# Kernel optimization log

Measured on AMD Instinct MI355X. Metric: run time of the kernel, lower is better.

The kernel has to match this reference:

```python
import jax, jax.numpy as jnp
import numpy as np

N_NODES = 100000
N_EDGES = 1200000
F_IN, F_HID, F_OUT = 128, 64, 40


def gcn_conv(x, W, b, src, dst, n):
    # PyG GCNConv: h = x @ W; add self-loops; symmetric norm; scatter-add; + bias
    h = x @ W  # [N, F]
    loops = jnp.arange(n)
    s = jnp.concatenate([src, loops])
    d = jnp.concatenate([dst, loops])
    deg = jnp.zeros((n,), x.dtype).at[d].add(jnp.asarray(1.0, x.dtype))
    dis = jax.lax.rsqrt(deg)  # deg >= 1 thanks to self-loops
    norm = dis[s] * dis[d]  # [E+N]
    msg = h[s] * norm[:, None]  # gather + scale
    out = jnp.zeros((n, h.shape[1]), x.dtype).at[d].add(msg)  # scatter-add
    return out + b


def setup_inputs() -> dict:
    key = jax.random.key(0)
    ks = jax.random.split(key, 8)
    sc = lambda f: 1.0 / np.sqrt(f)
    return {
        "x": jax.random.normal(ks[0], (N_NODES, F_IN), jnp.float32),
        "edge_index": jax.random.randint(ks[1], (2, N_EDGES), 0, N_NODES, jnp.int64),
        "W1": jax.random.normal(ks[2], (F_IN, F_HID), jnp.float32) * sc(F_IN),
        "b1": jnp.zeros((F_HID,), jnp.float32),
        "W2": jax.random.normal(ks[3], (F_HID, F_HID), jnp.float32) * sc(F_HID),
        "b2": jnp.zeros((F_HID,), jnp.float32),
        "W3": jax.random.normal(ks[4], (F_HID, F_OUT), jnp.float32) * sc(F_HID),
        "b3": jnp.zeros((F_OUT,), jnp.float32),
    }


def reference(x, edge_index, W1, b1, W2, b2, W3, b3):
    src, dst = edge_index[0], edge_index[1]
    n = x.shape[0]
    h = jax.nn.relu(gcn_conv(x, W1, b1, src, dst, n))  # dropout is identity (eval)
    h = jax.nn.relu(gcn_conv(h, W2, b2, src, dst, n))
    out = gcn_conv(h, W3, b3, src, dst, n)
    return jax.nn.log_softmax(out, axis=1)
```

## Files before the change

### kernel.cpp

```cpp
#include <hip/hip_runtime.h>
#include <math.h>


static inline int cdiv(long a, int b) { return (int)((a + b - 1) / b); }

__device__ __forceinline__ unsigned short f2bf(float f) {
    unsigned u = __float_as_uint(f);
    u += 0x7fffu + ((u >> 16) & 1u);
    return (unsigned short)(u >> 16);
}
__device__ __forceinline__ float bf2f(unsigned short b) {
    return __uint_as_float(((unsigned)b) << 16);
}

typedef float floatx2 __attribute__((ext_vector_type(2)));
typedef short bf16x8  __attribute__((ext_vector_type(8)));
typedef float f32x4   __attribute__((ext_vector_type(4)));
__device__ __forceinline__ float4 fp8x4_f(unsigned u) {
    floatx2 lo = __builtin_amdgcn_cvt_pk_f32_fp8(u, false);
    floatx2 hi = __builtin_amdgcn_cvt_pk_f32_fp8(u, true);
    float4 r; r.x = lo[0]; r.y = lo[1]; r.z = hi[0]; r.w = hi[1];
    return r;
}
__device__ __forceinline__ unsigned char f_fp8(float v) {
    return (unsigned char)(__builtin_amdgcn_cvt_pk_fp8_f32(v, v, 0u, false) & 0xFFu);
}

#define RSH 9
#define RNODES 512
#define GB 1024
#define NBMAX 256
#define SMASK 0x1FFFF
#define PSLACK (RNODES * 16)
#define EBMAX 12288

__global__ __launch_bounds__(256)
void k_bhist(const int* __restrict__ dst, int* __restrict__ bh,
             int E, int NB, int EPB) {
    __shared__ int bcnt[NBMAX];
    const int tid = threadIdx.x, blk = blockIdx.x;
    for (int i = tid; i < NB; i += 256) bcnt[i] = 0;
    __syncthreads();
    const int e1 = min(E, (blk + 1) * EPB);
    for (int e = blk * EPB + tid; e < e1; e += 256)
        atomicAdd(&bcnt[dst[e] >> RSH], 1);
    __syncthreads();
    for (int i = tid; i < NB; i += 256) bh[i * GB + blk] = bcnt[i];
}

__global__ __launch_bounds__(256)
void k_bscatter(const int* __restrict__ src, const int* __restrict__ dst,
                const int* __restrict__ eoff, int* __restrict__ ebuf,
                int E, int NB, int EPB) {
    __shared__ int cur[NBMAX];
    const int tid = threadIdx.x, blk = blockIdx.x;
    for (int i = tid; i < NB; i += 256) cur[i] = eoff[i * GB + blk];
    __syncthreads();
    const int e1 = min(E, (blk + 1) * EPB);
    for (int e = blk * EPB + tid; e < e1; e += 256) {
        int d = dst[e];
        int s = src[e];
        int pos = atomicAdd(&cur[d >> RSH], 1);
        ebuf[pos] = ((d & (RNODES - 1)) << 17) | s;
    }
}

__global__ __launch_bounds__(1024)
void k_csr(const int* __restrict__ ebuf, const int* __restrict__ eoff,
           uint2* __restrict__ rpd, float* __restrict__ dis,
           unsigned int* __restrict__ esrcb, int N, int E, int NB) {
    __shared__ int cnt[RNODES];
    __shared__ int cur[RNODES];
    __shared__ int sm[1024];
    __shared__ int esm[EBMAX];
    const int tid = threadIdx.x, b = blockIdx.x;
    const int node0 = b << RSH;
    const int bb = eoff[b * GB];
    const int be = (b + 1 == NB) ? E : eoff[(b + 1) * GB];
    const int nedge = be - bb;
    const bool inlds = (nedge <= EBMAX);
    const int pbase = ((bb + 15) & ~15) + b * PSLACK;

    if (tid < RNODES) cnt[tid] = 0;
    if (inlds) {
        for (int e = tid; e < nedge; e += 1024) esm[e] = ebuf[bb + e];
    }
    __syncthreads();
    for (int e = tid; e < nedge; e += 1024)
        atomicAdd(&cnt[(inlds ? esm[e] : ebuf[bb + e]) >> 17], 1);
    __syncthreads();

    int v  = (tid < RNODES) ? cnt[tid] : 0;
    int pv = (v + 15) & ~15;
    sm[tid] = pv;
    __syncthreads();
    for (int off = 1; off < RNODES; off <<= 1) {
        int t = (tid >= off) ? sm[tid - off] : 0;
        __syncthreads();
        sm[tid] += t;
        __syncthreads();
    }
    if (tid < RNODES) {
        int excl = sm[tid] - pv;
        cur[tid] = pbase + excl;
        int node = node0 + tid;
        if (node < N) {
            rpd[node] = make_uint2((unsigned)(pbase + excl), (unsigned)((v + 15) >> 4));
            dis[node] = rsqrtf(1.0f + (float)v);
        }
    }
    __syncthreads();

    for (int e = tid; e < nedge; e += 1024) {
        int ev = inlds ? esm[e] : ebuf[bb + e];
        int slot = atomicAdd(&cur[ev >> 17], 1);
        esrcb[slot] = (unsigned)(ev & SMASK) << 6;
    }
    __syncthreads();

    const unsigned ZOFF = (unsigned)N << 6;
    if (tid < RNODES) {
        const int end = pbase + sm[tid];
        for (int k = cur[tid]; k < end; ++k) esrcb[k] = ZOFF;
    }
}

#define SCAN_B 1024
__global__ void k_scan1(const int* __restrict__ cnt, int* __restrict__ rp,
                        int* __restrict__ bsum, int n, char* __restrict__ zbase,
                        int N) {
    __shared__ int sm[SCAN_B];
    const int tid = threadIdx.x;
    const int gid = blockIdx.x * SCAN_B + tid;
    if (blockIdx.x == 0 && tid < 16)
        ((unsigned*)(zbase + (size_t)N * 64))[tid] = 0;
    int v = (gid < n) ? cnt[gid] : 0;
    sm[tid] = v;
    __syncthreads();
    for (int off = 1; off < SCAN_B; off <<= 1) {
        int t = (tid >= off) ? sm[tid - off] : 0;
        __syncthreads();
        sm[tid] += t;
        __syncthreads();
    }
    if (gid < n) rp[gid] = sm[tid] - v;
    if (tid == SCAN_B - 1) bsum[blockIdx.x] = sm[tid];
}

__global__ void k_scan2(int* __restrict__ bsum, int nb) {
    __shared__ int sm[SCAN_B];
    const int tid = threadIdx.x;
    int v = (tid < nb) ? bsum[tid] : 0;
    sm[tid] = v;
    __syncthreads();
    for (int off = 1; off < SCAN_B; off <<= 1) {
        int t = (tid >= off) ? sm[tid - off] : 0;
        __syncthreads();
        sm[tid] += t;
        __syncthreads();
    }
    if (tid < nb) bsum[tid] = sm[tid] - v;
}

__global__ void k_scan3(int* __restrict__ rp, const int* __restrict__ bsum, int n, int E) {
    const int gid = blockIdx.x * SCAN_B + threadIdx.x;
    if (gid < n) rp[gid] += bsum[gid / SCAN_B];
    if (gid == n) rp[n] = E;
}

template<int K, bool BF16IN, int WCOLS, bool DIS>
__global__ __launch_bounds__(256, 4)
void k_mgemm(const void* __restrict__ Xv, const float* __restrict__ W,
             const float* __restrict__ dis, unsigned char* __restrict__ Hout, int N) {
    constexpr int KP = K + 8;
    __shared__ short xs[64 * KP];
    __shared__ short wt[64 * KP];
    const int tid = threadIdx.x;
    const int wv  = tid >> 6;
    const int l   = tid & 63;
    const int row0 = blockIdx.x * 64;

    for (int idx = tid; idx < K * 64; idx += 256) {
        int k = idx >> 6, n = idx & 63;
        float v;
        if (WCOLS == 64) v = W[k * 64 + n];
        else             v = (n < WCOLS) ? W[k * WCOLS + n] : 0.f;
        wt[n * KP + k] = (short)f2bf(v);
    }
    if (BF16IN) {
        constexpr int C4 = K / 4;
        for (int idx = tid; idx < 64 * C4; idx += 256) {
            int r = idx / C4, c = idx % C4;
            int gr = min(row0 + r, N - 1);
            ushort4 u = *(const ushort4*)((const unsigned short*)Xv + (size_t)gr * K + c * 4);
            *(ushort4*)(&xs[r * KP + c * 4]) = u;
        }
    } else {
        constexpr int C4 = K / 4;
        for (int idx = tid; idx < 64 * C4; idx += 256) {
            int r = idx / C4, c = idx % C4;
            int gr = min(row0 + r, N - 1);
            float4 v = *(const float4*)((const float*)Xv + (size_t)gr * K + c * 4);
            ushort4 u;
            u.x = f2bf(v.x); u.y = f2bf(v.y); u.z = f2bf(v.z); u.w = f2bf(v.w);
            *(ushort4*)(&xs[r * KP + c * 4]) = u;
        }
    }
    __syncthreads();

    f32x4 acc0 = {0.f, 0.f, 0.f, 0.f};
    f32x4 acc1 = {0.f, 0.f, 0.f, 0.f};
    f32x4 acc2 = {0.f, 0.f, 0.f, 0.f};
    f32x4 acc3 = {0.f, 0.f, 0.f, 0.f};
    const int arow = wv * 16 + (l & 15);
    const int koffl = (l >> 4) * 8;

#pragma unroll
    for (int ks = 0; ks < K; ks += 32) {
        bf16x8 a  = *(const bf16x8*)(&xs[arow * KP + ks + koffl]);
        bf16x8 b0 = *(const bf16x8*)(&wt[( 0 + (l & 15)) * KP + ks + koffl]);
        bf16x8 b1 = *(const bf16x8*)(&wt[(16 + (l & 15)) * KP + ks + koffl]);
        bf16x8 b2 = *(const bf16x8*)(&wt[(32 + (l & 15)) * KP + ks + koffl]);
        bf16x8 b3 = *(const bf16x8*)(&wt[(48 + (l & 15)) * KP + ks + koffl]);
        acc0 = __builtin_amdgcn_mfma_f32_16x16x32_bf16(a, b0, acc0, 0, 0, 0);
        acc1 = __builtin_amdgcn_mfma_f32_16x16x32_bf16(a, b1, acc1, 0, 0, 0);
        acc2 = __builtin_amdgcn_mfma_f32_16x16x32_bf16(a, b2, acc2, 0, 0, 0);
        acc3 = __builtin_amdgcn_mfma_f32_16x16x32_bf16(a, b3, acc3, 0, 0, 0);
    }

#pragma unroll
    for (int j = 0; j < 4; ++j) {
        int r = row0 + wv * 16 + ((l >> 4) << 2) + j;
        if (r < N) {
            float dd = DIS ? dis[r] : 1.0f;
            unsigned char* rowp = Hout + (size_t)r * 64 + (l & 15);
            rowp[0]  = f_fp8(acc0[j] * dd);
            rowp[16] = f_fp8(acc1[j] * dd);
            rowp[32] = f_fp8(acc2[j] * dd);
            rowp[48] = f_fp8(acc3[j] * dd);
        }
    }
}

template<int MODE>
__global__ __launch_bounds__(256, 8)
void k_agg(const unsigned char* __restrict__ Hs8, const float* __restrict__ dis,
           const uint2* __restrict__ rpd, const unsigned int* __restrict__ esrcb,
           const float* __restrict__ bias, void* __restrict__ A, int N) {
    const int wave = threadIdx.x >> 6;
    const int lane = threadIdx.x & 63;
    const int node = blockIdx.x * (blockDim.x >> 6) + wave;
    if (node >= N) return;
    const int q    = lane >> 4;
    const unsigned foff = (lane & 15) * 4;

    const uint2 pd = rpd[node];
    const char* base = (const char*)Hs8;
    floatx2 aL = {0.f, 0.f};
    floatx2 aH = {0.f, 0.f};
    unsigned e = pd.x + q * 4;
    for (unsigned it = 0; it < pd.y; ++it, e += 16) {
        uint4 ov = *(const uint4*)(esrcb + e);
        unsigned u0 = *(const unsigned*)(base + (ov.x + foff));
        unsigned u1 = *(const unsigned*)(base + (ov.y + foff));
        unsigned u2 = *(const unsigned*)(base + (ov.z + foff));
        unsigned u3 = *(const unsigned*)(base + (ov.w + foff));
        aL += __builtin_amdgcn_cvt_pk_f32_fp8(u0, false);
        aH += __builtin_amdgcn_cvt_pk_f32_fp8(u0, true);
        aL += __builtin_amdgcn_cvt_pk_f32_fp8(u1, false);
        aH += __builtin_amdgcn_cvt_pk_f32_fp8(u1, true);
        aL += __builtin_amdgcn_cvt_pk_f32_fp8(u2, false);
        aH += __builtin_amdgcn_cvt_pk_f32_fp8(u2, true);
        aL += __builtin_amdgcn_cvt_pk_f32_fp8(u3, false);
        aH += __builtin_amdgcn_cvt_pk_f32_fp8(u3, true);
    }
    float4 acc; acc.x = aL[0]; acc.y = aL[1]; acc.z = aH[0]; acc.w = aH[1];
    acc.x += __shfl_xor(acc.x, 16, 64);
    acc.y += __shfl_xor(acc.y, 16, 64);
    acc.z += __shfl_xor(acc.z, 16, 64);
    acc.w += __shfl_xor(acc.w, 16, 64);
    acc.x += __shfl_xor(acc.x, 32, 64);
    acc.y += __shfl_xor(acc.y, 32, 64);
    acc.z += __shfl_xor(acc.z, 32, 64);
    acc.w += __shfl_xor(acc.w, 32, 64);

    if (lane < 16) {
        const float dd = dis[node];
        unsigned shv = *(const unsigned*)(Hs8 + (size_t)node * 64 + lane * 4);
        float4 sh = fp8x4_f(shv);
        float4 v;
        v.x = (acc.x + sh.x) * dd;
        v.y = (acc.y + sh.y) * dd;
        v.z = (acc.z + sh.z) * dd;
        v.w = (acc.w + sh.w) * dd;
        float4 bv = ((const float4*)bias)[lane];
        v.x = fmaxf(v.x + bv.x, 0.f);
        v.y = fmaxf(v.y + bv.y, 0.f);
        v.z = fmaxf(v.z + bv.z, 0.f);
        v.w = fmaxf(v.w + bv.w, 0.f);
        if (MODE == 1) {
            v.x *= dd; v.y *= dd; v.z *= dd; v.w *= dd;
        }
        ushort4 o;
        o.x = f2bf(v.x); o.y = f2bf(v.y); o.z = f2bf(v.z); o.w = f2bf(v.w);
        *(ushort4*)((unsigned short*)A + (size_t)node * 64 + lane * 4) = o;
    }
}

__global__ __launch_bounds__(256, 8)
void k_aggz(const unsigned char* __restrict__ Z8, const float* __restrict__ dis,
            const uint2* __restrict__ rpd, const unsigned int* __restrict__ esrcb,
            const float* __restrict__ b3, float* __restrict__ out, int N) {
    const int wave = threadIdx.x >> 6;
    const int lane = threadIdx.x & 63;
    const int node = blockIdx.x * (blockDim.x >> 6) + wave;
    if (node >= N) return;
    const int q    = lane >> 4;
    const int f4   = lane & 15;
    const unsigned foff = f4 * 4;

    const uint2 pd = rpd[node];
    const char* base = (const char*)Z8;
    floatx2 aL = {0.f, 0.f};
    floatx2 aH = {0.f, 0.f};
    unsigned e = pd.x + q * 4;
    for (unsigned it = 0; it < pd.y; ++it, e += 16) {
        uint4 ov = *(const uint4*)(esrcb + e);
        unsigned u0 = *(const unsigned*)(base + (ov.x + foff));
        unsigned u1 = *(const unsigned*)(base + (ov.y + foff));
        unsigned u2 = *(const unsigned*)(base + (ov.z + foff));
        unsigned u3 = *(const unsigned*)(base + (ov.w + foff));
        aL += __builtin_amdgcn_cvt_pk_f32_fp8(u0, false);
        aH += __builtin_amdgcn_cvt_pk_f32_fp8(u0, true);
        aL += __builtin_amdgcn_cvt_pk_f32_fp8(u1, false);
        aH += __builtin_amdgcn_cvt_pk_f32_fp8(u1, true);
        aL += __builtin_amdgcn_cvt_pk_f32_fp8(u2, false);
        aH += __builtin_amdgcn_cvt_pk_f32_fp8(u2, true);
        aL += __builtin_amdgcn_cvt_pk_f32_fp8(u3, false);
        aH += __builtin_amdgcn_cvt_pk_f32_fp8(u3, true);
    }
    float4 acc; acc.x = aL[0]; acc.y = aL[1]; acc.z = aH[0]; acc.w = aH[1];
    acc.x += __shfl_xor(acc.x, 16, 64);
    acc.y += __shfl_xor(acc.y, 16, 64);
    acc.z += __shfl_xor(acc.z, 16, 64);
    acc.w += __shfl_xor(acc.w, 16, 64);
    acc.x += __shfl_xor(acc.x, 32, 64);
    acc.y += __shfl_xor(acc.y, 32, 64);
    acc.z += __shfl_xor(acc.z, 32, 64);
    acc.w += __shfl_xor(acc.w, 32, 64);

    const float dd = dis[node];
    unsigned shv = *(const unsigned*)(Z8 + (size_t)node * 64 + f4 * 4);
    float4 sh = fp8x4_f(shv);
    float4 bv = {0.f, 0.f, 0.f, 0.f};
    if (f4 < 10) bv = ((const float4*)b3)[f4];
    float4 v;
    v.x = (acc.x + sh.x) * dd + bv.x;
    v.y = (acc.y + sh.y) * dd + bv.y;
    v.z = (acc.z + sh.z) * dd + bv.z;
    v.w = (acc.w + sh.w) * dd + bv.w;

    float m = (f4 < 10) ? fmaxf(fmaxf(v.x, v.y), fmaxf(v.z, v.w)) : -INFINITY;
#pragma unroll
    for (int o = 1; o < 16; o <<= 1) m = fmaxf(m, __shfl_xor(m, o, 64));
    float es = (f4 < 10)
        ? expf(v.x - m) + expf(v.y - m) + expf(v.z - m) + expf(v.w - m) : 0.f;
#pragma unroll
    for (int o = 1; o < 16; o <<= 1) es += __shfl_xor(es, o, 64);

    if (lane < 10) {
        float ls = logf(es);
        float4 o4;
        o4.x = v.x - m - ls;
        o4.y = v.y - m - ls;
        o4.z = v.z - m - ls;
        o4.w = v.w - m - ls;
        *(float4*)(out + (size_t)node * 40 + lane * 4) = o4;
    }
}

extern "C" void kernel_launch(void* const* d_in, const int* in_sizes, int n_in,
                              void* d_out, int out_size, void* d_ws, size_t ws_size,
                              hipStream_t stream) {
    const float* x  = (const float*)d_in[0];
    const int*   ei = (const int*)d_in[1];
    const float* W1 = (const float*)d_in[2];
    const float* b1 = (const float*)d_in[3];
    const float* W2 = (const float*)d_in[4];
    const float* b2 = (const float*)d_in[5];
    const float* W3 = (const float*)d_in[6];
    const float* b3 = (const float*)d_in[7];
    float* out = (float*)d_out;

    const int N = in_sizes[0] / 128;
    const int E = in_sizes[1] / 2;
    const int* src = ei;
    const int* dst = ei + E;

    const int NB   = cdiv(N, RNODES);
    const int EPB  = cdiv(E, GB);
    const int nscan = NB * GB;
    const size_t esz = (size_t)E + (size_t)(NB + 2) * PSLACK + 64;

    char* ws = (char*)d_ws;
    char* buf0  = ws;                         ws += (size_t)(N + 1) * 64;
    char* buf1  = ws;                         ws += (size_t)N * 128;
    unsigned* esrcb = (unsigned*)ws;          ws += esz * sizeof(int);
    uint2* rpd  = (uint2*)ws;                 ws += (size_t)N * sizeof(uint2);
    int*   bsum  = (int*)ws;                  ws += (size_t)SCAN_B * sizeof(int);
    float* dis   = (float*)ws;                ws += (size_t)N * sizeof(float);
    int*   bh    = (int*)ws;                  ws += (size_t)nscan * sizeof(int);
    int*   eoff  = (int*)ws;                  ws += (size_t)(nscan + 1) * sizeof(int);
    int*   ebuf  = (int*)(ws);                ws += (size_t)E * sizeof(int);

    const int B = 256;
    const int nbs = cdiv(nscan, SCAN_B);
    const int ngb = cdiv(N, 64);

    k_bhist<<<GB, B, 0, stream>>>(dst, bh, E, NB, EPB);
    k_scan1<<<nbs, SCAN_B, 0, stream>>>(bh, eoff, bsum, nscan, buf0, N);
    k_scan2<<<1, SCAN_B, 0, stream>>>(bsum, nbs);
    k_scan3<<<cdiv(nscan + 1, SCAN_B), SCAN_B, 0, stream>>>(eoff, bsum, nscan, E);
    k_bscatter<<<GB, B, 0, stream>>>(src, dst, eoff, ebuf, E, NB, EPB);
    k_csr<<<NB, 1024, 0, stream>>>(ebuf, eoff, rpd, dis, esrcb, N, E, NB);

    k_mgemm<128, false, 64, true><<<ngb, B, 0, stream>>>(x, W1, dis,
                                                         (unsigned char*)buf0, N);
    k_agg<0><<<cdiv(N, 4), B, 0, stream>>>((const unsigned char*)buf0, dis, rpd, esrcb,
                                           b1, buf1, N);

    k_mgemm<64, true, 64, true><<<ngb, B, 0, stream>>>(buf1, W2, dis,
                                                       (unsigned char*)buf0, N);
    k_agg<1><<<cdiv(N, 4), B, 0, stream>>>((const unsigned char*)buf0, dis, rpd, esrcb,
                                           b2, buf1, N);

    k_mgemm<64, true, 40, false><<<ngb, B, 0, stream>>>(buf1, W3, dis,
                                                        (unsigned char*)buf0, N);
    k_aggz<<<cdiv(N, 4), B, 0, stream>>>((const unsigned char*)buf0, dis, rpd, esrcb,
                                         b3, out, N);
}
```

Before: 280.8 us.

## Locally sort edge chunks in LDS before bucket scatter; fold scan3 into consumers

k_bscatter now sorts each chunk of edges by destination bucket in shared memory and then writes contiguous runs per bucket to global memory, replacing random per-edge global stores. This is meant to coalesce the scatter writes. The scan3 kernel is removed, and the block offsets from bsum are added directly inside bscatter and csr, which saves a launch and a pass over the offsets. The agg kernels also hoist the dis, self-feature and bias loads ahead of the edge loop so they overlap with it. In exchange, bscatter gains extra barriers, a 256-step LDS scan per chunk, and more shared memory per block.

```diff
diff --git a/kernel.cpp b/kernel.cpp
--- a/kernel.cpp
+++ b/kernel.cpp
@@ -33,6 +33,7 @@
 #define SMASK 0x1FFFF
 #define PSLACK (RNODES * 16)
 #define EBMAX 12288
+#define EPBS 1280
 
 __global__ __launch_bounds__(256)
 void k_bhist(const int* __restrict__ dst, int* __restrict__ bh,
@@ -50,23 +51,70 @@
 
 __global__ __launch_bounds__(256)
 void k_bscatter(const int* __restrict__ src, const int* __restrict__ dst,
-                const int* __restrict__ eoff, int* __restrict__ ebuf,
-                int E, int NB, int EPB) {
-    __shared__ int cur[NBMAX];
+                const int* __restrict__ eoff, const int* __restrict__ bsum,
+                int* __restrict__ ebuf, int E, int NB, int EPB) {
+    __shared__ int hist[NBMAX];
+    __shared__ int lbase[NBMAX];
+    __shared__ int lcur[NBMAX];
+    __shared__ int gcur[NBMAX];
+    __shared__ int sm[NBMAX];
+    __shared__ int vals[EPBS];
+    __shared__ int sorted[EPBS];
+    __shared__ unsigned char bks[EPBS];
+    __shared__ unsigned char sbk[EPBS];
     const int tid = threadIdx.x, blk = blockIdx.x;
-    for (int i = tid; i < NB; i += 256) cur[i] = eoff[i * GB + blk];
-    __syncthreads();
-    const int e1 = min(E, (blk + 1) * EPB);
-    for (int e = blk * EPB + tid; e < e1; e += 256) {
-        int d = dst[e];
-        int s = src[e];
-        int pos = atomicAdd(&cur[d >> RSH], 1);
-        ebuf[pos] = ((d & (RNODES - 1)) << 17) | s;
+
+    for (int i = tid; i < NBMAX; i += 256)
+        gcur[i] = (i < NB) ? (eoff[i * GB + blk] + bsum[i]) : 0;
+
+    const int e0 = blk * EPB;
+    const int e1 = min(E, e0 + EPB);
+    for (int ch = e0; ch < e1; ch += EPBS) {
+        const int n = min(e1 - ch, EPBS);
+        for (int i = tid; i < NBMAX; i += 256) hist[i] = 0;
+        __syncthreads();
+        for (int i = tid; i < n; i += 256) {
+            int d = dst[ch + i];
+            int s = src[ch + i];
+            int bk = d >> RSH;
+            vals[i] = ((d & (RNODES - 1)) << 17) | s;
+            bks[i]  = (unsigned char)bk;
+            atomicAdd(&hist[bk], 1);
+        }
+        __syncthreads();
+        int hv = hist[tid];
+        sm[tid] = hv;
+        __syncthreads();
+        for (int off = 1; off < NBMAX; off <<= 1) {
+            int t = (tid >= off) ? sm[tid - off] : 0;
+            __syncthreads();
+            sm[tid] += t;
+            __syncthreads();
+        }
+        lbase[tid] = sm[tid] - hv;
+        lcur[tid] = 0;
+        __syncthreads();
+        for (int i = tid; i < n; i += 256) {
+            int bk = bks[i];
+            int r = atomicAdd(&lcur[bk], 1);
+            int p = lbase[bk] + r;
+            sorted[p] = vals[i];
+            sbk[p] = (unsigned char)bk;
+        }
+        __syncthreads();
+        for (int j = tid; j < n; j += 256) {
+            int bk = sbk[j];
+            ebuf[gcur[bk] + (j - lbase[bk])] = sorted[j];
+        }
+        __syncthreads();
+        for (int i = tid; i < NBMAX; i += 256) gcur[i] += hist[i];
+        __syncthreads();
     }
 }
 
 __global__ __launch_bounds__(1024)
 void k_csr(const int* __restrict__ ebuf, const int* __restrict__ eoff,
+           const int* __restrict__ bsum,
            uint2* __restrict__ rpd, float* __restrict__ dis,
            unsigned int* __restrict__ esrcb, int N, int E, int NB) {
     __shared__ int cnt[RNODES];
@@ -75,8 +123,8 @@
     __shared__ int esm[EBMAX];
     const int tid = threadIdx.x, b = blockIdx.x;
     const int node0 = b << RSH;
-    const int bb = eoff[b * GB];
-    const int be = (b + 1 == NB) ? E : eoff[(b + 1) * GB];
+    const int bb = eoff[b * GB] + bsum[b];
+    const int be = (b + 1 == NB) ? E : (eoff[(b + 1) * GB] + bsum[b + 1]);
     const int nedge = be - bb;
     const bool inlds = (nedge <= EBMAX);
     const int pbase = ((bb + 15) & ~15) + b * PSLACK;
@@ -162,12 +210,6 @@
     if (tid < nb) bsum[tid] = sm[tid] - v;
 }
 
-__global__ void k_scan3(int* __restrict__ rp, const int* __restrict__ bsum, int n, int E) {
-    const int gid = blockIdx.x * SCAN_B + threadIdx.x;
-    if (gid < n) rp[gid] += bsum[gid / SCAN_B];
-    if (gid == n) rp[n] = E;
-}
-
 template<int K, bool BF16IN, int WCOLS, bool DIS>
 __global__ __launch_bounds__(256, 4)
 void k_mgemm(const void* __restrict__ Xv, const float* __restrict__ W,
@@ -252,9 +294,14 @@
     const int node = blockIdx.x * (blockDim.x >> 6) + wave;
     if (node >= N) return;
     const int q    = lane >> 4;
-    const unsigned foff = (lane & 15) * 4;
+    const int f4   = lane & 15;
+    const unsigned foff = f4 * 4;
 
     const uint2 pd = rpd[node];
+    const float dd = dis[node];
+    unsigned shv = *(const unsigned*)(Hs8 + (size_t)node * 64 + foff);
+    float4 bv = ((const float4*)bias)[f4];
+
     const char* base = (const char*)Hs8;
     floatx2 aL = {0.f, 0.f};
     floatx2 aH = {0.f, 0.f};
@@ -285,15 +332,12 @@
     acc.w += __shfl_xor(acc.w, 32, 64);
 
     if (lane < 16) {
-        const float dd = dis[node];
-        unsigned shv = *(const unsigned*)(Hs8 + (size_t)node * 64 + lane * 4);
         float4 sh = fp8x4_f(shv);
         float4 v;
         v.x = (acc.x + sh.x) * dd;
         v.y = (acc.y + sh.y) * dd;
         v.z = (acc.z + sh.z) * dd;
         v.w = (acc.w + sh.w) * dd;
-        float4 bv = ((const float4*)bias)[lane];
         v.x = fmaxf(v.x + bv.x, 0.f);
         v.y = fmaxf(v.y + bv.y, 0.f);
         v.z = fmaxf(v.z + bv.z, 0.f);
@@ -320,6 +364,10 @@
     const unsigned foff = f4 * 4;
 
     const uint2 pd = rpd[node];
+    const float dd = dis[node];
+    unsigned shv = *(const unsigned*)(Z8 + (size_t)node * 64 + foff);
+    float4 bv = ((const float4*)b3)[min(f4, 9)];
+
     const char* base = (const char*)Z8;
     floatx2 aL = {0.f, 0.f};
     floatx2 aH = {0.f, 0.f};
@@ -349,11 +397,7 @@
     acc.z += __shfl_xor(acc.z, 32, 64);
     acc.w += __shfl_xor(acc.w, 32, 64);
 
-    const float dd = dis[node];
-    unsigned shv = *(const unsigned*)(Z8 + (size_t)node * 64 + f4 * 4);
     float4 sh = fp8x4_f(shv);
-    float4 bv = {0.f, 0.f, 0.f, 0.f};
-    if (f4 < 10) bv = ((const float4*)b3)[f4];
     float4 v;
     v.x = (acc.x + sh.x) * dd + bv.x;
     v.y = (acc.y + sh.y) * dd + bv.y;
@@ -420,9 +464,8 @@
     k_bhist<<<GB, B, 0, stream>>>(dst, bh, E, NB, EPB);
     k_scan1<<<nbs, SCAN_B, 0, stream>>>(bh, eoff, bsum, nscan, buf0, N);
     k_scan2<<<1, SCAN_B, 0, stream>>>(bsum, nbs);
-    k_scan3<<<cdiv(nscan + 1, SCAN_B), SCAN_B, 0, stream>>>(eoff, bsum, nscan, E);
-    k_bscatter<<<GB, B, 0, stream>>>(src, dst, eoff, ebuf, E, NB, EPB);
-    k_csr<<<NB, 1024, 0, stream>>>(ebuf, eoff, rpd, dis, esrcb, N, E, NB);
+    k_bscatter<<<GB, B, 0, stream>>>(src, dst, eoff, bsum, ebuf, E, NB, EPB);
+    k_csr<<<NB, 1024, 0, stream>>>(ebuf, eoff, bsum, rpd, dis, esrcb, N, E, NB);
 
     k_mgemm<128, false, 64, true><<<ngb, B, 0, stream>>>(x, W1, dis,
                                                          (unsigned char*)buf0, N);
```

Result: faster. 270.6 us (-3.6%).
